# Kernel optimization log

Hardware: AMD Instinct MI355X
Metric: run time of the kernel (lower is better)

Reference implementation:

```python
import jax, jax.numpy as jnp
import numpy as np
from jax import lax

DN = ('NCHW', 'OIHW', 'NCHW')


def squash(x):
    # x: [..., d]; squared-norm over last dim
    sq = jnp.sum(x * x, axis=-1, keepdims=True)
    return sq * x / ((1.0 + sq) * jnp.sqrt(sq))


def setup_inputs() -> dict:
    key = jax.random.key(0)
    ks = jax.random.split(key, 6)
    B = 512
    x = jax.random.normal(ks[0], (B, 1, 28, 28), dtype=jnp.float32)
    conv1_w = jax.random.normal(ks[1], (256, 1, 9, 9), dtype=jnp.float32) * 0.05
    conv1_b = jnp.zeros((256,), dtype=jnp.float32)
    conv2_w = jax.random.normal(ks[2], (256, 256, 9, 9), dtype=jnp.float32) * 0.02
    conv2_b = jnp.zeros((256,), dtype=jnp.float32)
    # W: [num_routes=1152, num_capsules=10, out_channels=16, in_channels=8]
    W = jax.random.normal(ks[3], (1152, 10, 16, 8), dtype=jnp.float32)
    return {"x": x, "conv1_w": conv1_w, "conv1_b": conv1_b,
            "conv2_w": conv2_w, "conv2_b": conv2_b, "W": W}


def reference(x, conv1_w, conv1_b, conv2_w, conv2_b, W):
    B = x.shape[0]
    # conv1 + ReLU: [B,1,28,28] -> [B,256,20,20]
    h = lax.conv_general_dilated(x, conv1_w, (1, 1), 'VALID', dimension_numbers=DN)
    h = jax.nn.relu(h + conv1_b[None, :, None, None])
    # primary capsule conv: [B,256,20,20] -> [B,256,6,6], stride 2
    h = lax.conv_general_dilated(h, conv2_w, (2, 2), 'VALID', dimension_numbers=DN)
    h = h + conv2_b[None, :, None, None]
    # reshape to capsules [B, 1152, 8] (matches torch .view on NCHW) and squash
    u = squash(h.reshape(B, -1, 8))
    # u_hat[b,r,c,o] = W[r,c,o,i] @ u[b,r,i]
    u_hat = jnp.einsum('rcoi,bri->brco', W, u)  # [B,1152,10,16]
    R, C = W.shape[0], W.shape[1]
    b_ij = jnp.zeros((R, C), dtype=x.dtype)
    num_iterations = 3
    for it in range(num_iterations):
        c_ij = jax.nn.softmax(b_ij, axis=0)          # softmax over routes
        s_j = jnp.einsum('rc,brco->bco', c_ij, u_hat)  # [B,10,16]
        v_j = squash(s_j)
        if it < num_iterations - 1:
            a_ij = jnp.einsum('brco,bco->brc', u_hat, v_j)  # agreement
            b_ij = b_ij + a_ij.mean(axis=0)
    return v_j  # [B,10,16]
```

## Files before the change

kernel.cpp:

```cpp
#include <hip/hip_runtime.h>
#include <stdint.h>


typedef unsigned short u16;
typedef unsigned int u32;
typedef _Float16 half8 __attribute__((ext_vector_type(8)));
typedef float f32x4 __attribute__((ext_vector_type(4)));

__device__ __forceinline__ u16 f2h(float f) {
  union { _Float16 h; u16 u; } cv;
  cv.h = (_Float16)f;
  return cv.u;
}

__device__ __forceinline__ void gload_lds16(const void* g, void* l) {
  __builtin_amdgcn_global_load_lds(
      (const __attribute__((address_space(1))) void*)g,
      (__attribute__((address_space(3))) void*)l, 16, 0, 0);
}

__global__ __launch_bounds__(256) void prologue_kernel(
    const float* __restrict__ x, const float* __restrict__ w1,
    const float* __restrict__ b1, const float* __restrict__ w2,
    const float* __restrict__ b2, u16* __restrict__ hT,
    u16* __restrict__ A2, float* __restrict__ u) {
  __shared__ __align__(16) char smraw[81 * 264 * 2];
  int bid = blockIdx.x;
  int tid = threadIdx.x;
  if (bid < 1024) {
    float* xs = (float*)smraw;
    int b = bid >> 1, half = bid & 1;
    int co = tid;
    const float* xbase = x + (size_t)b * 784 + half * 280;
    for (int i = co; i < 504; i += 256) xs[i] = xbase[i];
    float w[81];
    const float* wp = w1 + co * 81;
#pragma unroll
    for (int k = 0; k < 81; ++k) w[k] = wp[k];
    float bias = b1[co];
    __syncthreads();
    u16* hb = hT + (size_t)b * 102400 + co;
    for (int yp = 0; yp < 5; ++yp) {
      int y0l = yp * 2;
      int y0g = half * 10 + y0l;
      for (int g = 0; g < 5; ++g) {
        int xo = g * 4;
        float a0[4], a1[4];
#pragma unroll
        for (int j = 0; j < 4; ++j) { a0[j] = bias; a1[j] = bias; }
#pragma unroll
        for (int ky2 = 0; ky2 < 10; ++ky2) {
          const float* row = &xs[(y0l + ky2) * 28 + xo];
          float4 r0 = *(const float4*)row;
          float4 r1 = *(const float4*)(row + 4);
          float4 r2 = *(const float4*)(row + 8);
          float xr[12] = {r0.x, r0.y, r0.z, r0.w, r1.x, r1.y, r1.z, r1.w,
                          r2.x, r2.y, r2.z, r2.w};
          if (ky2 < 9) {
#pragma unroll
            for (int kx = 0; kx < 9; ++kx) {
              float wv = w[ky2 * 9 + kx];
              a0[0] = fmaf(wv, xr[kx], a0[0]);
              a0[1] = fmaf(wv, xr[kx + 1], a0[1]);
              a0[2] = fmaf(wv, xr[kx + 2], a0[2]);
              a0[3] = fmaf(wv, xr[kx + 3], a0[3]);
            }
          }
          if (ky2 >= 1) {
#pragma unroll
            for (int kx = 0; kx < 9; ++kx) {
              float wv = w[(ky2 - 1) * 9 + kx];
              a1[0] = fmaf(wv, xr[kx], a1[0]);
              a1[1] = fmaf(wv, xr[kx + 1], a1[1]);
              a1[2] = fmaf(wv, xr[kx + 2], a1[2]);
              a1[3] = fmaf(wv, xr[kx + 3], a1[3]);
            }
          }
        }
#pragma unroll
        for (int j = 0; j < 4; ++j) {
          hb[(y0g * 20 + xo + j) * 256] = f2h(fmaxf(a0[j], 0.f));
          hb[((y0g + 1) * 20 + xo + j) * 256] = f2h(fmaxf(a1[j], 0.f));
        }
      }
    }
  } else if (bid < 1280) {
    u16* tl = (u16*)smraw;
    int co = bid - 1024;
    const float* wp = w2 + (size_t)co * 20736;
#pragma unroll
    for (int k = 0; k < 81; ++k) {
      int li = k * 256 + tid;
      int ci = li / 81, t = li - ci * 81;
      tl[t * 264 + ci] = f2h(wp[li]);
    }
    __syncthreads();
    u16* op = A2 + (size_t)co * 20736;
    for (int oc = tid; oc < 2592; oc += 256) {
      int k0 = oc * 8;
      int t = k0 >> 8, ci0 = k0 & 255;
      *(uint4*)(op + k0) = *(const uint4*)&tl[t * 264 + ci0];
    }
  } else {
    int i = (bid - 1280) * 256 + tid;
    int b = i / 2304, j0 = (i - b * 2304) * 4;
    float4 v;
    v.x = b2[j0 / 36]; v.y = b2[(j0 + 1) / 36];
    v.z = b2[(j0 + 2) / 36]; v.w = b2[(j0 + 3) / 36];
    *(float4*)(u + (size_t)b * 9216 + j0) = v;
  }
}

__global__ __launch_bounds__(1024, 4) void conv2_kernel(
    const u16* __restrict__ hT, const u16* __restrict__ A2,
    float* __restrict__ u) {
  __shared__ __align__(16) u16 lds_[65536];
  char* const ldsc = (char*)lds_;
  const int bx = blockIdx.x;
  const int nbk = bx % 72, kz = bx / 72;
  const int n0 = nbk * 256;
  const int tid = threadIdx.x;
  const int lane = tid & 63, w = tid >> 6;
  const int wr = w >> 2, wc = w & 3;
  const int fr = lane & 15, fg = lane >> 4;
  const int w1024 = w * 1024;

  const int rA = tid >> 3;
  const int qs = (tid & 7) ^ (rA & 7);
  const int Aoff0 = rA * 20736 + qs * 8;
  const int Aoff1 = (128 + rA) * 20736 + qs * 8;
  int Bb0, Bb1;
  {
    int n = n0 + rA;
    int b = n / 36, sp = n - b * 36, oh = sp / 6, ow = sp - oh * 6;
    Bb0 = (b * 400 + oh * 40 + ow * 2) * 256 + qs * 8;
    n = n0 + 128 + rA;
    b = n / 36; sp = n - b * 36; oh = sp / 6; ow = sp - oh * 6;
    Bb1 = (b * 400 + oh * 40 + ow * 2) * 256 + qs * 8;
  }

  const int kx0 = (fg ^ (fr & 7)) << 4;
  const int kx1 = ((4 + fg) ^ (fr & 7)) << 4;
  const int arow = wr * 64 + fr;
  const int brow = wc * 64 + fr;

  f32x4 acc[4][4] = {};
  half8 areg[4], breg[4];

#define STAGE4(E, GT) do {                                                   \
    int tap_ = (GT) >> 2;                                                    \
    int kh_ = tap_ / 9, kw_ = tap_ - kh_ * 9;                                \
    int bo_ = (kh_ * 20 + kw_) * 256 + ((GT) & 3) * 64;                      \
    char* base_ = ldsc + (E) * 65536;                                        \
    gload_lds16(A2 + Aoff0 + (GT) * 64, base_ + w1024);                      \
    gload_lds16(A2 + Aoff1 + (GT) * 64, base_ + 16384 + w1024);              \
    gload_lds16(hT + Bb0 + bo_, base_ + 32768 + w1024);                      \
    gload_lds16(hT + Bb1 + bo_, base_ + 49152 + w1024);                      \
  } while (0)
#define RD8(D, KX) do { _Pragma("unroll")                                    \
    for (int mr = 0; mr < 4; ++mr)                                           \
      areg[mr] = *(const half8*)(ldsc + (D) * 65536 +                        \
                                 (arow + mr * 16) * 128 + (KX));             \
    _Pragma("unroll")                                                        \
    for (int nr = 0; nr < 4; ++nr)                                           \
      breg[nr] = *(const half8*)(ldsc + (D) * 65536 + 32768 +                \
                                 (brow + nr * 16) * 128 + (KX));             \
  } while (0)
#define MM16() do {                                                          \
    __builtin_amdgcn_s_setprio(1);                                           \
    _Pragma("unroll") for (int mr = 0; mr < 4; ++mr)                         \
    _Pragma("unroll") for (int nr = 0; nr < 4; ++nr)                         \
      acc[mr][nr] = __builtin_amdgcn_mfma_f32_16x16x32_f16(                  \
          areg[mr], breg[nr], acc[mr][nr], 0, 0, 0);                         \
    __builtin_amdgcn_s_setprio(0);                                           \
  } while (0)
#define LGKM() do {                                                          \
    asm volatile("s_waitcnt lgkmcnt(0)" ::: "memory");                       \
    __builtin_amdgcn_sched_barrier(0);                                       \
  } while (0)
#define VM_BAR0() do {                                                       \
    asm volatile("s_waitcnt vmcnt(0)" ::: "memory");                         \
    __builtin_amdgcn_s_barrier();                                            \
    asm volatile("" ::: "memory");                                           \
  } while (0)
#define TILE_STD(T, D, E) do {                                               \
    RD8(D, kx0);                                                             \
    STAGE4(E, kz * 108 + (T) + 1);                                           \
    LGKM(); MM16();                                                          \
    RD8(D, kx1); LGKM(); MM16();                                             \
    VM_BAR0();                                                               \
  } while (0)
#define TILE_LAST(D) do {                                                    \
    RD8(D, kx0); LGKM(); MM16();                                             \
    RD8(D, kx1); LGKM(); MM16();                                             \
  } while (0)

  STAGE4(0, kz * 108);
  asm volatile("s_waitcnt vmcnt(0)" ::: "memory");
  __builtin_amdgcn_s_barrier();
  asm volatile("" ::: "memory");

  for (int tt = 0; tt < 53; ++tt) {
    TILE_STD(2 * tt, 0, 1);
    TILE_STD(2 * tt + 1, 1, 0);
  }
  TILE_STD(106, 0, 1);
  TILE_LAST(1);

#pragma unroll
  for (int nf = 0; nf < 4; ++nf) {
    int cn = n0 + wc * 64 + nf * 16 + fr;
    int ob = cn / 36;
    int os = cn - ob * 36;
    float* op = u + (size_t)ob * 9216 + os;
#pragma unroll
    for (int mf = 0; mf < 4; ++mf) {
      int row0 = wr * 64 + mf * 16 + fg * 4;
#pragma unroll
      for (int qq = 0; qq < 4; ++qq)
        atomicAdd(op + (row0 + qq) * 36, acc[mf][nf][qq]);
    }
  }
#undef STAGE4
#undef RD8
#undef MM16
#undef LGKM
#undef VM_BAR0
#undef TILE_STD
#undef TILE_LAST
}

__global__ __launch_bounds__(256) void squash_kernel(
    float* __restrict__ u, u16* __restrict__ ub) {
  int idx = blockIdx.x * 256 + threadIdx.x;
  float* up = u + (size_t)idx * 8;
  float4 a = *(const float4*)up;
  float4 c = *(const float4*)(up + 4);
  float sq = a.x * a.x + a.y * a.y + a.z * a.z + a.w * a.w +
             c.x * c.x + c.y * c.y + c.z * c.z + c.w * c.w;
  float f = sqrtf(sq) / (1.0f + sq);
  a.x *= f; a.y *= f; a.z *= f; a.w *= f;
  c.x *= f; c.y *= f; c.z *= f; c.w *= f;
  *(float4*)up = a;
  *(float4*)(up + 4) = c;
  u16 o[8];
  o[0] = f2h(a.x); o[1] = f2h(a.y); o[2] = f2h(a.z); o[3] = f2h(a.w);
  o[4] = f2h(c.x); o[5] = f2h(c.y); o[6] = f2h(c.z); o[7] = f2h(c.w);
  *(uint4*)(ub + (size_t)idx * 8) = *(uint4*)o;
}

__global__ __launch_bounds__(256) void transp_kernel(
    const u16* __restrict__ ub, u16* __restrict__ ubT) {
  __shared__ u16 tl[64][72];
  int ri0 = blockIdx.x * 64, b0 = blockIdx.y * 64;
  int tid = threadIdx.x;
  int br = tid >> 2, cq = tid & 3;
  const u16* ip = ub + (size_t)(b0 + br) * 9216 + ri0 + cq * 16;
  uint4 v0 = *(const uint4*)ip;
  uint4 v1 = *(const uint4*)(ip + 8);
  *(uint4*)&tl[br][cq * 16] = v0;
  *(uint4*)&tl[br][cq * 16 + 8] = v1;
  __syncthreads();
  int rr = tid >> 2, cb = tid & 3;
  u16 o0[8], o1[8];
#pragma unroll
  for (int j = 0; j < 8; ++j) {
    o0[j] = tl[cb * 16 + j][rr];
    o1[j] = tl[cb * 16 + 8 + j][rr];
  }
  u16* opp = ubT + (size_t)(ri0 + rr) * 512 + b0 + cb * 16;
  *(uint4*)opp = *(uint4*)o0;
  *(uint4*)(opp + 8) = *(uint4*)o1;
}

__global__ __launch_bounds__(256) void softmax_c_kernel(
    const float* __restrict__ bij, float* __restrict__ cT) {
  int c = blockIdx.x;
  int tid = threadIdx.x;
  __shared__ float red[256];
  float mx = -1e30f;
  for (int r = tid; r < 1152; r += 256) mx = fmaxf(mx, bij[r * 10 + c]);
  red[tid] = mx;
  __syncthreads();
  for (int s = 128; s > 0; s >>= 1) {
    if (tid < s) red[tid] = fmaxf(red[tid], red[tid + s]);
    __syncthreads();
  }
  mx = red[0];
  __syncthreads();
  float sum = 0.f;
  for (int r = tid; r < 1152; r += 256) sum += expf(bij[r * 10 + c] - mx);
  red[tid] = sum;
  __syncthreads();
  for (int s = 128; s > 0; s >>= 1) {
    if (tid < s) red[tid] += red[tid + s];
    __syncthreads();
  }
  float inv = 1.0f / red[0];
  for (int r = tid; r < 1152; r += 256)
    cT[c * 1152 + r] = expf(bij[r * 10 + c] - mx) * inv;
}

__global__ __launch_bounds__(256) void gemm_s_kernel(
    const float* __restrict__ W, const float* __restrict__ cT,
    const u16* __restrict__ ub, float* __restrict__ s) {
  __shared__ __align__(16) u16 Asl[160 * 72];
  __shared__ __align__(16) u16 Bsl[64 * 72];
  int nb = blockIdx.x & 7, kzi = blockIdx.x >> 3;
  int n0 = nb * 64, k0 = kzi * 256;
  int tid = threadIdx.x;
  int lane = tid & 63, wave = tid >> 6;
  int fr = lane & 15, fg = lane >> 4;

  f32x4 acc[10] = {};
#pragma unroll
  for (int st = 0; st < 4; ++st) {
    int kb = k0 + st * 64;
    __syncthreads();
#pragma unroll
    for (int j = 0; j < 5; ++j) {
      int c5 = tid + j * 256;
      int row = c5 >> 3, qq = c5 & 7;
      int cls = row >> 4, o = row & 15;
      int r = (kb + qq * 8) >> 3;
      const float* wp = W + (size_t)r * 1280 + cls * 128 + o * 8;
      float4 w0 = *(const float4*)wp;
      float4 w1 = *(const float4*)(wp + 4);
      float cs = cT[cls * 1152 + r] * 512.0f;
      u16 ov[8];
      ov[0] = f2h(w0.x * cs); ov[1] = f2h(w0.y * cs);
      ov[2] = f2h(w0.z * cs); ov[3] = f2h(w0.w * cs);
      ov[4] = f2h(w1.x * cs); ov[5] = f2h(w1.y * cs);
      ov[6] = f2h(w1.z * cs); ov[7] = f2h(w1.w * cs);
      *(uint4*)((char*)Asl + row * 144 + qq * 16) = *(uint4*)ov;
    }
#pragma unroll
    for (int j = 0; j < 2; ++j) {
      int c2 = tid + j * 256;
      int row = c2 >> 3, qq = c2 & 7;
      *(uint4*)((char*)Bsl + row * 144 + qq * 16) =
          *(const uint4*)(ub + (size_t)(n0 + row) * 9216 + kb + qq * 8);
    }
    __syncthreads();
#pragma unroll
    for (int s2 = 0; s2 < 2; ++s2) {
      int xg = (s2 * 4 + fg) * 16;
      half8 bf0 = *(const half8*)((char*)Bsl + (wave * 16 + fr) * 144 + xg);
#pragma unroll
      for (int m = 0; m < 10; ++m) {
        half8 af = *(const half8*)((char*)Asl + (m * 16 + fr) * 144 + xg);
        acc[m] = __builtin_amdgcn_mfma_f32_16x16x32_f16(af, bf0, acc[m], 0, 0, 0);
      }
    }
  }
  int bcol = n0 + wave * 16 + fr;
#pragma unroll
  for (int m = 0; m < 10; ++m)
#pragma unroll
    for (int qq = 0; qq < 4; ++qq)
      atomicAdd(s + (m * 16 + fg * 4 + qq) * 512 + bcol, acc[m][qq]);
}

__global__ __launch_bounds__(256) void squash_v_kernel(
    float* __restrict__ s, u16* __restrict__ vb) {
  int idx = blockIdx.x * 256 + threadIdx.x;
  int c = idx >> 9, b = idx & 511;
  float vals[16];
  float sq = 0.f;
#pragma unroll
  for (int o = 0; o < 16; ++o) {
    float v = s[(c * 16 + o) * 512 + b] * (1.0f / 512.0f);
    vals[o] = v;
    sq += v * v;
  }
#pragma unroll
  for (int o = 0; o < 16; ++o) s[(c * 16 + o) * 512 + b] = 0.f;
  float f = sqrtf(sq) / (1.0f + sq);
#pragma unroll
  for (int o = 0; o < 16; ++o)
    vb[(c * 16 + o) * 512 + b] = f2h(vals[o] * f * 4096.0f);
}

__global__ __launch_bounds__(256) void gemm_gc_kernel(
    const u16* __restrict__ vb, const u16* __restrict__ ubT,
    const float* __restrict__ W, float* __restrict__ bij) {
  __shared__ __align__(16) u16 Agl[160 * 72];
  __shared__ __align__(16) u16 Bgl[128 * 72];
  __shared__ float Gl[160 * 129];
  int nb = blockIdx.x % 72, kzi = blockIdx.x / 72;
  int n0 = nb * 128, k0 = kzi * 128;
  int tid = threadIdx.x;
  int lane = tid & 63, wave = tid >> 6;
  int fr = lane & 15, fg = lane >> 4;
  f32x4 acc[10][2] = {};
#pragma unroll
  for (int st = 0; st < 2; ++st) {
    int kb = k0 + st * 64;
    __syncthreads();
#pragma unroll
    for (int j = 0; j < 5; ++j) {
      int c5 = tid + j * 256;
      int row = c5 >> 3, qq = c5 & 7;
      *(uint4*)((char*)Agl + row * 144 + qq * 16) =
          *(const uint4*)(vb + (size_t)row * 512 + kb + qq * 8);
    }
#pragma unroll
    for (int j = 0; j < 4; ++j) {
      int c4 = tid + j * 256;
      int row = c4 >> 3, qq = c4 & 7;
      *(uint4*)((char*)Bgl + row * 144 + qq * 16) =
          *(const uint4*)(ubT + (size_t)(n0 + row) * 512 + kb + qq * 8);
    }
    __syncthreads();
#pragma unroll
    for (int s2 = 0; s2 < 2; ++s2) {
      int xg = (s2 * 4 + fg) * 16;
      half8 bfv[2];
#pragma unroll
      for (int nn = 0; nn < 2; ++nn)
        bfv[nn] = *(const half8*)((char*)Bgl + (wave * 32 + nn * 16 + fr) * 144 + xg);
#pragma unroll
      for (int m = 0; m < 10; ++m) {
        half8 af = *(const half8*)((char*)Agl + (m * 16 + fr) * 144 + xg);
#pragma unroll
        for (int nn = 0; nn < 2; ++nn)
          acc[m][nn] = __builtin_amdgcn_mfma_f32_16x16x32_f16(af, bfv[nn],
                                                             acc[m][nn], 0, 0, 0);
      }
    }
  }
#pragma unroll
  for (int m = 0; m < 10; ++m)
#pragma unroll
    for (int nn = 0; nn < 2; ++nn) {
      int col = wave * 32 + nn * 16 + fr;
#pragma unroll
      for (int qq = 0; qq < 4; ++qq)
        Gl[(m * 16 + fg * 4 + qq) * 129 + col] = acc[m][nn][qq];
    }
  __syncthreads();
  if (tid < 160) {
    int rl = tid / 10, c = tid - rl * 10;
    int r = (n0 >> 3) + rl;
    const float* wp = W + (size_t)r * 1280 + c * 128;
    float a = 0.f;
#pragma unroll 4
    for (int o = 0; o < 16; ++o) {
      const float* gp = &Gl[(c * 16 + o) * 129 + rl * 8];
#pragma unroll
      for (int i = 0; i < 8; ++i) a = fmaf(wp[o * 8 + i], gp[i], a);
    }
    atomicAdd(&bij[r * 10 + c], a * (1.0f / (512.0f * 4096.0f)));
  }
}

__global__ __launch_bounds__(256) void route_final_kernel(
    const float* __restrict__ cT, const float* __restrict__ u,
    const float* __restrict__ W, float* __restrict__ outp) {
  int c = blockIdx.y, b0 = blockIdx.x * 16;
  int tid = threadIdx.x, lb = tid >> 4, o = tid & 15;
  __shared__ float us[16][32][8];
  __shared__ float cs[32];
  float acc = 0.f;
  for (int r0 = 0; r0 < 1152; r0 += 32) {
    __syncthreads();
#pragma unroll
    for (int j = 0; j < 4; ++j) {
      int i4 = tid + j * 256;
      int bb = i4 >> 6, rem = i4 & 63;
      int rr = rem >> 1, hf = rem & 1;
      *(float4*)&us[bb][rr][hf * 4] =
          *(const float4*)&u[(size_t)(b0 + bb) * 9216 + (r0 + rr) * 8 + hf * 4];
    }
    if (tid < 32) cs[tid] = cT[c * 1152 + r0 + tid];
    __syncthreads();
#pragma unroll 4
    for (int rr = 0; rr < 32; ++rr) {
      const float* wp = W + ((size_t)(r0 + rr) * 10 + c) * 128 + o * 8;
      float4 w0 = *(const float4*)wp;
      float4 w1v = *(const float4*)(wp + 4);
      float4 ua = *(const float4*)&us[lb][rr][0];
      float4 ub4 = *(const float4*)&us[lb][rr][4];
      float d = w0.x * ua.x + w0.y * ua.y + w0.z * ua.z + w0.w * ua.w +
                w1v.x * ub4.x + w1v.y * ub4.y + w1v.z * ub4.z + w1v.w * ub4.w;
      acc = fmaf(cs[rr], d, acc);
    }
  }
  float sq = acc * acc;
  sq += __shfl_xor(sq, 1, 64);
  sq += __shfl_xor(sq, 2, 64);
  sq += __shfl_xor(sq, 4, 64);
  sq += __shfl_xor(sq, 8, 64);
  float f = sqrtf(sq) / (1.0f + sq);
  outp[((size_t)(b0 + lb) * 10 + c) * 16 + o] = acc * f;
}

extern "C" void kernel_launch(void* const* d_in, const int* in_sizes, int n_in,
                              void* d_out, int out_size, void* d_ws, size_t ws_size,
                              hipStream_t stream) {
  const float* x  = (const float*)d_in[0];
  const float* w1 = (const float*)d_in[1];
  const float* b1 = (const float*)d_in[2];
  const float* w2 = (const float*)d_in[3];
  const float* b2 = (const float*)d_in[4];
  const float* W  = (const float*)d_in[5];
  char* ws = (char*)d_ws;
  u16*   hT  = (u16*)ws;
  u16*   A2  = (u16*)(ws + 104857600);
  float* u   = (float*)(ws + 115474432);
  float* bij = (float*)(ws + 134348800);
  float* cT  = (float*)(ws + 134394880);
  float* s   = (float*)(ws + 134440960);
  u16*   ub  = (u16*)ws;
  u16*   ubT = (u16*)(ws + 9437184);
  u16*   vb  = (u16*)(ws + 21823488);
  float* out = (float*)d_out;

  hipMemsetAsync(bij, 0, 46080, stream);
  hipMemsetAsync(s, 0, 327680, stream);
  prologue_kernel<<<5888, 256, 0, stream>>>(x, w1, b1, w2, b2, hT, A2, u);
  conv2_kernel<<<216, 1024, 0, stream>>>(hT, A2, u);
  squash_kernel<<<2304, 256, 0, stream>>>(u, ub);
  transp_kernel<<<dim3(144, 8), 256, 0, stream>>>(ub, ubT);
  for (int it = 0; it < 3; ++it) {
    softmax_c_kernel<<<10, 256, 0, stream>>>(bij, cT);
    if (it < 2) {
      gemm_s_kernel<<<288, 256, 0, stream>>>(W, cT, ub, s);
      squash_v_kernel<<<20, 256, 0, stream>>>(s, vb);
      gemm_gc_kernel<<<288, 256, 0, stream>>>(vb, ubT, W, bij);
    } else {
      route_final_kernel<<<dim3(32, 10), 256, 0, stream>>>(cT, u, W, out);
    }
  }
}
```

Measured before the change: 616.4 us.

## Fuse memsets into prologue, merge squash with transpose, split routing GEMMs finer

```diff
diff --git a/kernel.cpp b/kernel.cpp
--- a/kernel.cpp
+++ b/kernel.cpp
@@ -23,7 +23,8 @@
     const float* __restrict__ x, const float* __restrict__ w1,
     const float* __restrict__ b1, const float* __restrict__ w2,
     const float* __restrict__ b2, u16* __restrict__ hT,
-    u16* __restrict__ A2, float* __restrict__ u) {
+    u16* __restrict__ A2, float* __restrict__ u,
+    float* __restrict__ bij, float* __restrict__ s) {
   __shared__ __align__(16) char smraw[81 * 264 * 2];
   int bid = blockIdx.x;
   int tid = threadIdx.x;
@@ -101,13 +102,20 @@
       int t = k0 >> 8, ci0 = k0 & 255;
       *(uint4*)(op + k0) = *(const uint4*)&tl[t * 264 + ci0];
     }
-  } else {
+  } else if (bid < 5888) {
     int i = (bid - 1280) * 256 + tid;
     int b = i / 2304, j0 = (i - b * 2304) * 4;
     float4 v;
     v.x = b2[j0 / 36]; v.y = b2[(j0 + 1) / 36];
     v.z = b2[(j0 + 2) / 36]; v.w = b2[(j0 + 3) / 36];
     *(float4*)(u + (size_t)b * 9216 + j0) = v;
+  } else {
+    int i4 = (bid - 5888) * 256 + tid;
+    if (i4 < 23360) {
+      float4 z = make_float4(0.f, 0.f, 0.f, 0.f);
+      if (i4 < 2880) *(float4*)(bij + i4 * 4) = z;
+      else *(float4*)(s + (i4 - 2880) * 4) = z;
+    }
   }
 }
 
@@ -230,45 +238,41 @@
 #undef TILE_LAST
 }
 
-__global__ __launch_bounds__(256) void squash_kernel(
-    float* __restrict__ u, u16* __restrict__ ub) {
-  int idx = blockIdx.x * 256 + threadIdx.x;
-  float* up = u + (size_t)idx * 8;
-  float4 a = *(const float4*)up;
-  float4 c = *(const float4*)(up + 4);
-  float sq = a.x * a.x + a.y * a.y + a.z * a.z + a.w * a.w +
-             c.x * c.x + c.y * c.y + c.z * c.z + c.w * c.w;
-  float f = sqrtf(sq) / (1.0f + sq);
-  a.x *= f; a.y *= f; a.z *= f; a.w *= f;
-  c.x *= f; c.y *= f; c.z *= f; c.w *= f;
-  *(float4*)up = a;
-  *(float4*)(up + 4) = c;
-  u16 o[8];
-  o[0] = f2h(a.x); o[1] = f2h(a.y); o[2] = f2h(a.z); o[3] = f2h(a.w);
-  o[4] = f2h(c.x); o[5] = f2h(c.y); o[6] = f2h(c.z); o[7] = f2h(c.w);
-  *(uint4*)(ub + (size_t)idx * 8) = *(uint4*)o;
-}
-
-__global__ __launch_bounds__(256) void transp_kernel(
-    const u16* __restrict__ ub, u16* __restrict__ ubT) {
+__global__ __launch_bounds__(256) void squashT_kernel(
+    float* __restrict__ u, u16* __restrict__ ub, u16* __restrict__ ubT) {
   __shared__ u16 tl[64][72];
   int ri0 = blockIdx.x * 64, b0 = blockIdx.y * 64;
+  int r0 = ri0 >> 3;
   int tid = threadIdx.x;
-  int br = tid >> 2, cq = tid & 3;
-  const u16* ip = ub + (size_t)(b0 + br) * 9216 + ri0 + cq * 16;
-  uint4 v0 = *(const uint4*)ip;
-  uint4 v1 = *(const uint4*)(ip + 8);
-  *(uint4*)&tl[br][cq * 16] = v0;
-  *(uint4*)&tl[br][cq * 16 + 8] = v1;
+#pragma unroll
+  for (int hcap = 0; hcap < 2; ++hcap) {
+    int cap = hcap * 256 + tid;
+    int bb = cap >> 3, rr = cap & 7;
+    float* up = u + (size_t)(b0 + bb) * 9216 + (r0 + rr) * 8;
+    float4 a = *(const float4*)up;
+    float4 c = *(const float4*)(up + 4);
+    float sq = a.x * a.x + a.y * a.y + a.z * a.z + a.w * a.w +
+               c.x * c.x + c.y * c.y + c.z * c.z + c.w * c.w;
+    float f = sqrtf(sq) / (1.0f + sq);
+    a.x *= f; a.y *= f; a.z *= f; a.w *= f;
+    c.x *= f; c.y *= f; c.z *= f; c.w *= f;
+    *(float4*)up = a;
+    *(float4*)(up + 4) = c;
+    u16 o[8];
+    o[0] = f2h(a.x); o[1] = f2h(a.y); o[2] = f2h(a.z); o[3] = f2h(a.w);
+    o[4] = f2h(c.x); o[5] = f2h(c.y); o[6] = f2h(c.z); o[7] = f2h(c.w);
+    *(uint4*)(ub + (size_t)(b0 + bb) * 9216 + (r0 + rr) * 8) = *(uint4*)o;
+    *(uint4*)&tl[bb][rr * 8] = *(uint4*)o;
+  }
   __syncthreads();
-  int rr = tid >> 2, cb = tid & 3;
+  int rr2 = tid >> 2, cb = tid & 3;
   u16 o0[8], o1[8];
 #pragma unroll
   for (int j = 0; j < 8; ++j) {
-    o0[j] = tl[cb * 16 + j][rr];
-    o1[j] = tl[cb * 16 + 8 + j][rr];
-  }
-  u16* opp = ubT + (size_t)(ri0 + rr) * 512 + b0 + cb * 16;
+    o0[j] = tl[cb * 16 + j][rr2];
+    o1[j] = tl[cb * 16 + 8 + j][rr2];
+  }
+  u16* opp = ubT + (size_t)(ri0 + rr2) * 512 + b0 + cb * 16;
   *(uint4*)opp = *(uint4*)o0;
   *(uint4*)(opp + 8) = *(uint4*)o1;
 }
@@ -307,14 +311,14 @@
   __shared__ __align__(16) u16 Asl[160 * 72];
   __shared__ __align__(16) u16 Bsl[64 * 72];
   int nb = blockIdx.x & 7, kzi = blockIdx.x >> 3;
-  int n0 = nb * 64, k0 = kzi * 256;
+  int n0 = nb * 64, k0 = kzi * 128;
   int tid = threadIdx.x;
   int lane = tid & 63, wave = tid >> 6;
   int fr = lane & 15, fg = lane >> 4;
 
   f32x4 acc[10] = {};
 #pragma unroll
-  for (int st = 0; st < 4; ++st) {
+  for (int st = 0; st < 2; ++st) {
     int kb = k0 + st * 64;
     __syncthreads();
 #pragma unroll
@@ -388,15 +392,12 @@
   __shared__ __align__(16) u16 Bgl[128 * 72];
   __shared__ float Gl[160 * 129];
   int nb = blockIdx.x % 72, kzi = blockIdx.x / 72;
-  int n0 = nb * 128, k0 = kzi * 128;
+  int n0 = nb * 128, kb = kzi * 64;
   int tid = threadIdx.x;
   int lane = tid & 63, wave = tid >> 6;
   int fr = lane & 15, fg = lane >> 4;
   f32x4 acc[10][2] = {};
-#pragma unroll
-  for (int st = 0; st < 2; ++st) {
-    int kb = k0 + st * 64;
-    __syncthreads();
+  {
 #pragma unroll
     for (int j = 0; j < 5; ++j) {
       int c5 = tid + j * 256;
@@ -516,18 +517,15 @@
   u16*   vb  = (u16*)(ws + 21823488);
   float* out = (float*)d_out;
 
-  hipMemsetAsync(bij, 0, 46080, stream);
-  hipMemsetAsync(s, 0, 327680, stream);
-  prologue_kernel<<<5888, 256, 0, stream>>>(x, w1, b1, w2, b2, hT, A2, u);
+  prologue_kernel<<<5980, 256, 0, stream>>>(x, w1, b1, w2, b2, hT, A2, u, bij, s);
   conv2_kernel<<<216, 1024, 0, stream>>>(hT, A2, u);
-  squash_kernel<<<2304, 256, 0, stream>>>(u, ub);
-  transp_kernel<<<dim3(144, 8), 256, 0, stream>>>(ub, ubT);
+  squashT_kernel<<<dim3(144, 8), 256, 0, stream>>>(u, ub, ubT);
   for (int it = 0; it < 3; ++it) {
     softmax_c_kernel<<<10, 256, 0, stream>>>(bij, cT);
     if (it < 2) {
-      gemm_s_kernel<<<288, 256, 0, stream>>>(W, cT, ub, s);
+      gemm_s_kernel<<<576, 256, 0, stream>>>(W, cT, ub, s);
       squash_v_kernel<<<20, 256, 0, stream>>>(s, vb);
-      gemm_gc_kernel<<<288, 256, 0, stream>>>(vb, ubT, W, bij);
+      gemm_gc_kernel<<<576, 256, 0, stream>>>(vb, ubT, W, bij);
     } else {
       route_final_kernel<<<dim3(32, 10), 256, 0, stream>>>(cT, u, W, out);
     }
```

Result: no change. 612.2 us (-0.7%).
